# Kernel optimization log

Hardware: AMD Instinct MI355X
Metric: run time of the kernel (lower is better)

Reference implementation:

```python
import jax, jax.numpy as jnp
import numpy as np

DIM = 128
SQRT_DIM = float(np.sqrt(DIM))


def setup_inputs() -> dict:
    key = jax.random.key(0)
    k1, k2, k3, k4 = jax.random.split(key, 4)
    B, S, D = 16, 2048, DIM
    return {
        "query": jax.random.normal(k1, (B, S, D), dtype=jnp.float32),
        "key": jax.random.normal(k2, (B, S, D), dtype=jnp.float32),
        "value": jax.random.normal(k3, (B, S, D), dtype=jnp.float32),
        "trust_score": jax.random.uniform(k4, (B, 1, S), dtype=jnp.float32, minval=0.05, maxval=1.0),
    }


def reference(query, key, value, trust_score):
    # score: [B, q, k]
    score = jnp.einsum("bqd,bkd->bqk", query, key) / SQRT_DIM
    score = score * trust_score
    attn = jax.nn.softmax(score, axis=-1)
    # trust reweighting + renormalization
    attn = attn * trust_score
    attn = attn / jnp.sum(attn, axis=-1, keepdims=True)
    context = jnp.einsum("bqk,bkd->bqd", attn, value)
    return context
```

## Files before the change

kernel.cpp:

```cpp
#include <hip/hip_runtime.h>
#include <math.h>

#define SEQ 2048
#define DIM 128
#define KVB 32
#define NTILES (SEQ / KVB)
#define NT2 (NTILES / 2)
#define KTB 8192
#define VTB 8192

typedef __attribute__((ext_vector_type(8))) short bf16x8;
typedef __attribute__((ext_vector_type(16))) float f32x16;
typedef __attribute__((ext_vector_type(4))) short short4v;
typedef __attribute__((ext_vector_type(4))) float f32x4;

union frag_u { bf16x8 h; unsigned u[4]; };

__device__ __forceinline__ short f2bf(float f) {
  union { float f; unsigned u; } v; v.f = f;
  unsigned r = v.u + 0x7FFFu + ((v.u >> 16) & 1u);
  return (short)(r >> 16);
}
__device__ __forceinline__ float bf2f(short h) {
  return __uint_as_float(((unsigned)(unsigned short)h) << 16);
}
__device__ __forceinline__ void dma16(const void* g, void* l) {
  __builtin_amdgcn_global_load_lds(
      (const __attribute__((address_space(1))) void*)g,
      (__attribute__((address_space(3))) void*)l, 16, 0, 0);
}
__device__ __forceinline__ unsigned cvtpk(float lo, float hi) {
  unsigned r;
  asm("v_cvt_pk_bf16_f32 %0, %1, %2" : "=v"(r) : "v"(lo), "v"(hi));
  return r;
}
__device__ __forceinline__ void pl32swap(unsigned& a, unsigned& b) {
  asm("v_permlane32_swap_b32 %0, %1" : "+v"(a), "+v"(b));
}

__global__ __launch_bounds__(256)
void prepack_kernel(const float* __restrict__ Kg, const float* __restrict__ Vg,
                    const float* __restrict__ Tg,
                    char* __restrict__ Kws, char* __restrict__ Vws,
                    unsigned* __restrict__ Lws) {
  const int tile = blockIdx.x, b = blockIdx.y;
  const int tid = (int)threadIdx.x;
  const float* Kb = Kg + ((size_t)b * SEQ + tile * KVB) * DIM;
  const float* Vb = Vg + ((size_t)b * SEQ + tile * KVB) * DIM;
  const float* Tb = Tg + (size_t)b * SEQ + tile * KVB;
  char* kd = Kws + (size_t)(b * NTILES + tile) * KTB;
  char* vd = Vws + (size_t)(b * NTILES + tile) * VTB;

  #pragma unroll
  for (int i = 0; i < 2; ++i) {
    int id = i * 256 + tid;
    int k = id >> 4, c16 = id & 15;
    float sc = Tb[k] * 0.12751743f;
    const float4 f0 = *(const float4*)(Kb + (size_t)k * DIM + c16 * 8);
    const float4 f1 = *(const float4*)(Kb + (size_t)k * DIM + c16 * 8 + 4);
    bf16x8 pk;
    pk[0]=f2bf(f0.x*sc); pk[1]=f2bf(f0.y*sc); pk[2]=f2bf(f0.z*sc); pk[3]=f2bf(f0.w*sc);
    pk[4]=f2bf(f1.x*sc); pk[5]=f2bf(f1.y*sc); pk[6]=f2bf(f1.z*sc); pk[7]=f2bf(f1.w*sc);
    *(bf16x8*)(kd + k * 256 + ((c16 ^ (k & 7) ^ ((k >> 3) & 3)) << 4)) = pk;
  }
  #pragma unroll
  for (int i = 0; i < 2; ++i) {
    int id = i * 256 + tid;
    int d = id & 127, ch = id >> 7;
    const float* src = Vb + (size_t)(ch * 8) * DIM + d;
    bf16x8 pk;
    #pragma unroll
    for (int j = 0; j < 8; ++j) pk[j] = f2bf(src[(size_t)j * DIM]);
    *(bf16x8*)(vd + d * 64 + ((ch ^ ((d >> 1) & 3) ^ ((d >> 3) & 3)) << 4)) = pk;
  }
  if (tid < KVB) {
    float t = Tb[tid];
    float lt = log2f(t);
    short h = f2bf(lt);
    short lo = f2bf(lt - bf2f(h));
    Lws[(size_t)b * SEQ + tile * KVB + tid] =
        (unsigned)(unsigned short)h | ((unsigned)(unsigned short)lo << 16);
  }
}

__global__ __launch_bounds__(256, 2)
void trust_attn_main(const float* __restrict__ Qg, const char* __restrict__ Kws,
                     const char* __restrict__ Vws, const unsigned* __restrict__ Lws,
                     float* __restrict__ Og, int swz) {
  __shared__ __align__(16) char smem[65536];

  const int bid = (int)blockIdx.x;
  int b, qblk;
  if (swz) { int xcd = bid & 7, idx = bid >> 3; b = xcd * 2 + (idx >> 5); qblk = idx & 31; }
  else     { b = bid >> 5; qblk = bid & 31; }

  const int tid = (int)threadIdx.x;
  const int h   = tid >> 7;
  const int gq  = (tid >> 6) & 1;
  const int l   = tid & 63;
  const int hi  = l >> 5, l31 = l & 31;
  const int t128 = tid & 127;
  const int qcol = qblk * 64 + gq * 32 + l31;

  const float* Qr = Qg + ((size_t)b * SEQ + qcol) * DIM;
  const char* Kt = Kws + (size_t)(b * NTILES + h * NT2) * KTB;
  const char* Vt = Vws + (size_t)(b * NTILES + h * NT2) * VTB;
  const unsigned* Lb = Lws + (size_t)b * SEQ + h * (NT2 * KVB);

  frag_u qf[8];
  #pragma unroll
  for (int c = 0; c < 8; ++c) {
    const float4 a = *(const float4*)(Qr + c * 16 + hi * 8);
    const float4 d = *(const float4*)(Qr + c * 16 + hi * 8 + 4);
    bf16x8 q8;
    q8[0]=f2bf(a.x); q8[1]=f2bf(a.y); q8[2]=f2bf(a.z); q8[3]=f2bf(a.w);
    q8[4]=f2bf(d.x); q8[5]=f2bf(d.y); q8[6]=f2bf(d.z); q8[7]=f2bf(d.w);
    qf[c].h = q8;
  }
  frag_u qpad;
  qpad.u[0] = (hi == 0) ? 0x3F803F80u : 0u;
  qpad.u[1] = qpad.u[2] = qpad.u[3] = 0u;

  f32x16 acc[4];
  #pragma unroll
  for (int nt = 0; nt < 4; ++nt)
    #pragma unroll
    for (int i = 0; i < 16; ++i) acc[nt][i] = 0.f;
  float lsum = 0.f;

  auto ISSUE = [&](int t, int buf) {
    const char* ks = Kt + (size_t)t * KTB;
    const char* vs = Vt + (size_t)t * VTB;
    char* kl = smem + (h * 2 + buf) * 8192;
    char* vl = smem + 32768 + (h * 2 + buf) * 8192;
    #pragma unroll
    for (int j = 0; j < 2; ++j) {
      dma16(ks + j * 4096 + t128 * 16, kl + j * 4096 + t128 * 16);
      dma16(ks + j * 4096 + 2048 + t128 * 16, kl + j * 4096 + 2048 + t128 * 16);
      dma16(vs + j * 4096 + t128 * 16, vl + j * 4096 + t128 * 16);
      dma16(vs + j * 4096 + 2048 + t128 * 16, vl + j * 4096 + 2048 + t128 * 16);
    }
  };

  ISSUE(0, 0);
  unsigned ltc = Lb[l31];
  __syncthreads();

  for (int t = 0; t < NT2; ++t) {
    const int cur = t & 1;
    unsigned ltn = 0;
    if (t + 1 < NT2) {
      ISSUE(t + 1, cur ^ 1);
      ltn = Lb[(t + 1) * KVB + l31];
    }

    const char* Kc = smem + (h * 2 + cur) * 8192;
    const char* Vc = smem + 32768 + (h * 2 + cur) * 8192;

    f32x16 S0, S1;
    #pragma unroll
    for (int i = 0; i < 16; ++i) { S0[i] = 0.f; S1[i] = 0.f; }
    __builtin_amdgcn_s_setprio(1);
    #pragma unroll
    for (int c = 0; c < 8; c += 2) {
      frag_u kf0, kf1;
      kf0.h = *(const bf16x8*)(Kc + l31 * 256 + (((2 * c + hi) ^ (l31 & 7) ^ ((l31 >> 3) & 3)) << 4));
      kf1.h = *(const bf16x8*)(Kc + l31 * 256 + (((2 * (c + 1) + hi) ^ (l31 & 7) ^ ((l31 >> 3) & 3)) << 4));
      S0 = __builtin_amdgcn_mfma_f32_32x32x16_bf16(kf0.h, qf[c].h, S0, 0, 0, 0);
      S1 = __builtin_amdgcn_mfma_f32_32x32x16_bf16(kf1.h, qf[c + 1].h, S1, 0, 0, 0);
    }
    frag_u pa;
    pa.u[0] = (hi == 0) ? ltc : 0u;
    pa.u[1] = pa.u[2] = pa.u[3] = 0u;
    S1 = __builtin_amdgcn_mfma_f32_32x32x16_bf16(pa.h, qpad.h, S1, 0, 0, 0);
    __builtin_amdgcn_s_setprio(0);

    float p[16];
    #pragma unroll
    for (int i = 0; i < 16; ++i) {
      p[i] = __builtin_amdgcn_exp2f(S0[i] + S1[i]);
      lsum += p[i];
    }

    frag_u PA[2];
    #pragma unroll
    for (int ks = 0; ks < 2; ++ks) {
      unsigned a0 = cvtpk(p[8*ks+0], p[8*ks+1]);
      unsigned a1 = cvtpk(p[8*ks+2], p[8*ks+3]);
      unsigned b0 = cvtpk(p[8*ks+4], p[8*ks+5]);
      unsigned b1 = cvtpk(p[8*ks+6], p[8*ks+7]);
      pl32swap(a0, b0);
      pl32swap(a1, b1);
      PA[ks].u[0] = a0; PA[ks].u[1] = a1; PA[ks].u[2] = b0; PA[ks].u[3] = b1;
    }

    __builtin_amdgcn_s_setprio(1);
    #pragma unroll
    for (int nt = 0; nt < 4; ++nt)
      #pragma unroll
      for (int ks = 0; ks < 2; ++ks) {
        frag_u vf;
        vf.h = *(const bf16x8*)(Vc + (nt * 32 + l31) * 64 +
                (((2 * ks + hi) ^ ((l31 >> 1) & 3) ^ ((l31 >> 3) & 3)) << 4));
        acc[nt] = __builtin_amdgcn_mfma_f32_32x32x16_bf16(vf.h, PA[ks].h, acc[nt], 0, 0, 0);
      }
    __builtin_amdgcn_s_setprio(0);

    ltc = ltn;
    __syncthreads();
  }

  const float Z = lsum + __shfl_xor(lsum, 32);
  float* AccX = (float*)smem;
  float* Zx   = (float*)(smem + 32768);
  const int q2 = gq * 32 + l31;

  if (h == 1) {
    if (hi == 0) Zx[q2] = Z;
    #pragma unroll
    for (int nt = 0; nt < 4; ++nt)
      #pragma unroll
      for (int j = 0; j < 4; ++j) {
        int d = nt * 32 + j * 8 + hi * 4;
        int byte_off = (q2 * 512 + d * 4) ^ ((l31 & 7) << 4);
        f32x4 qd;
        qd[0] = acc[nt][j*4+0]; qd[1] = acc[nt][j*4+1];
        qd[2] = acc[nt][j*4+2]; qd[3] = acc[nt][j*4+3];
        *(f32x4*)((char*)AccX + byte_off) = qd;
      }
  }
  __syncthreads();
  if (h == 0) {
    const float inv = 1.0f / (Z + Zx[q2]);
    float* orow = Og + ((size_t)b * SEQ + qcol) * DIM;
    #pragma unroll
    for (int nt = 0; nt < 4; ++nt)
      #pragma unroll
      for (int j = 0; j < 4; ++j) {
        int d = nt * 32 + j * 8 + hi * 4;
        int byte_off = (q2 * 512 + d * 4) ^ ((l31 & 7) << 4);
        f32x4 o = *(const f32x4*)((const char*)AccX + byte_off);
        float4 r;
        r.x = (acc[nt][j*4+0] + o[0]) * inv;
        r.y = (acc[nt][j*4+1] + o[1]) * inv;
        r.z = (acc[nt][j*4+2] + o[2]) * inv;
        r.w = (acc[nt][j*4+3] + o[3]) * inv;
        *(float4*)(orow + d) = r;
      }
  }
}

__global__ __launch_bounds__(256, 2)
void trust_attn_fallback(const float* __restrict__ Qg, const float* __restrict__ Kg,
                         const float* __restrict__ Vg, const float* __restrict__ Tg,
                         float* __restrict__ Og) {
  __shared__ short Klds[2][64 * DIM];
  __shared__ short Vlds[2][DIM * 64];
  __shared__ short Plds[4][16 * 64];
  __shared__ float Tlds[2][64];

  const int b = blockIdx.y;
  const int qbase = blockIdx.x * 64;
  const int tid = (int)threadIdx.x;
  const int w = tid >> 6;
  const int l = tid & 63;
  const int lr = l & 15;
  const int lg = l >> 4;

  const float* Qb = Qg + (size_t)b * SEQ * DIM;
  const float* Kb = Kg + (size_t)b * SEQ * DIM;
  const float* Vb = Vg + (size_t)b * SEQ * DIM;
  const float* Tb = Tg + (size_t)b * SEQ;
  float*       Ob = Og + (size_t)b * SEQ * DIM;

  float4 kreg[8];
  float  vreg[32];
  float  treg;

  auto ISSUE = [&](int kv0) {
    #pragma unroll
    for (int i = 0; i < 8; ++i) {
      int flat4 = i * 256 + tid;
      int r = flat4 >> 5;
      int c4 = (flat4 & 31) << 2;
      kreg[i] = *(const float4*)(Kb + (size_t)(kv0 + r) * DIM + c4);
    }
    #pragma unroll
    for (int i = 0; i < 4; ++i) {
      int task = i * 256 + tid;
      int d = task & 127;
      int chunk = task >> 7;
      const float* src = Vb + (size_t)(kv0 + chunk * 8) * DIM + d;
      #pragma unroll
      for (int j = 0; j < 8; ++j) vreg[i * 8 + j] = src[(size_t)j * DIM];
    }
    treg = (tid < 64) ? Tb[kv0 + tid] : 0.f;
  };

  auto STORE = [&](int buf) {
    #pragma unroll
    for (int i = 0; i < 8; ++i) {
      int flat4 = i * 256 + tid;
      int r = flat4 >> 5;
      int c4 = (flat4 & 31) << 2;
      short4v pk;
      pk[0] = f2bf(kreg[i].x); pk[1] = f2bf(kreg[i].y);
      pk[2] = f2bf(kreg[i].z); pk[3] = f2bf(kreg[i].w);
      int byte_off = (r * 256 + (c4 << 1)) ^ ((r & 7) << 4);
      *(short4v*)((char*)&Klds[buf][0] + byte_off) = pk;
    }
    #pragma unroll
    for (int i = 0; i < 4; ++i) {
      int task = i * 256 + tid;
      int d = task & 127;
      int chunk = task >> 7;
      bf16x8 pk;
      #pragma unroll
      for (int j = 0; j < 8; ++j) pk[j] = f2bf(vreg[i * 8 + j]);
      int byte_off = (d * 128 + chunk * 16) ^ ((d & 7) << 4);
      *(bf16x8*)((char*)&Vlds[buf][0] + byte_off) = pk;
    }
    if (tid < 64) Tlds[buf][tid] = treg;
  };

  bf16x8 qf[4];
  {
    const float* qrow = Qb + (size_t)(qbase + w * 16 + lr) * DIM;
    #pragma unroll
    for (int kk = 0; kk < 4; ++kk) {
      const float4 a = *(const float4*)(qrow + kk * 32 + lg * 8);
      const float4 c = *(const float4*)(qrow + kk * 32 + lg * 8 + 4);
      bf16x8 f;
      f[0] = f2bf(a.x); f[1] = f2bf(a.y); f[2] = f2bf(a.z); f[3] = f2bf(a.w);
      f[4] = f2bf(c.x); f[5] = f2bf(c.y); f[6] = f2bf(c.z); f[7] = f2bf(c.w);
      qf[kk] = f;
    }
  }

  f32x4 acc[8];
  #pragma unroll
  for (int nt = 0; nt < 8; ++nt) acc[nt] = f32x4{0.f, 0.f, 0.f, 0.f};
  float lsum[4] = {0.f, 0.f, 0.f, 0.f};

  ISSUE(0);
  STORE(0);
  __syncthreads();

  for (int t = 0; t < SEQ / 64; ++t) {
    const int cur = t & 1;
    if (t + 1 < SEQ / 64) ISSUE((t + 1) * 64);

    const short* Kc = &Klds[cur][0];
    const short* Vc = &Vlds[cur][0];

    f32x4 s[4];
    #pragma unroll
    for (int kt = 0; kt < 4; ++kt) {
      f32x4 a0 = f32x4{0.f, 0.f, 0.f, 0.f};
      #pragma unroll
      for (int kk = 0; kk < 4; ++kk) {
        int row = kt * 16 + lr;
        int byte_off = (row * 256 + ((kk * 32 + lg * 8) << 1)) ^ ((row & 7) << 4);
        bf16x8 kf = *(const bf16x8*)((const char*)Kc + byte_off);
        a0 = __builtin_amdgcn_mfma_f32_16x16x32_bf16(qf[kk], kf, a0, 0, 0, 0);
      }
      s[kt] = a0;
    }

    short* Pw = Plds[w];
    #pragma unroll
    for (int kt = 0; kt < 4; ++kt) {
      float tt = Tlds[cur][kt * 16 + lr];
      float tc = tt * 0.12751743f;
      #pragma unroll
      for (int r = 0; r < 4; ++r) {
        float p = tt * exp2f(s[kt][r] * tc);
        lsum[r] += p;
        int q = lg * 4 + r;
        int byte_off = ((q * 128) + ((kt * 16 + lr) << 1)) ^ ((q & 7) << 4);
        *(short*)((char*)Pw + byte_off) = f2bf(p);
      }
    }
    asm volatile("s_waitcnt lgkmcnt(0)" ::: "memory");

    #pragma unroll
    for (int ks = 0; ks < 2; ++ks) {
      int byteA = (lr * 128 + ((ks * 32 + lg * 8) << 1)) ^ ((lr & 7) << 4);
      bf16x8 pf = *(const bf16x8*)((char*)Pw + byteA);
      #pragma unroll
      for (int nt = 0; nt < 8; ++nt) {
        int row = nt * 16 + lr;
        int byteB = (row * 128 + ((ks * 32 + lg * 8) << 1)) ^ ((row & 7) << 4);
        bf16x8 vf = *(const bf16x8*)((const char*)Vc + byteB);
        acc[nt] = __builtin_amdgcn_mfma_f32_16x16x32_bf16(pf, vf, acc[nt], 0, 0, 0);
      }
    }

    if (t + 1 < SEQ / 64) {
      STORE(cur ^ 1);
      __syncthreads();
    }
  }

  #pragma unroll
  for (int r = 0; r < 4; ++r) {
    float v = lsum[r];
    v += __shfl_xor(v, 1);
    v += __shfl_xor(v, 2);
    v += __shfl_xor(v, 4);
    v += __shfl_xor(v, 8);
    float inv = 1.0f / v;
    float* dst = Ob + (size_t)(qbase + w * 16 + lg * 4 + r) * DIM + lr;
    #pragma unroll
    for (int nt = 0; nt < 8; ++nt)
      dst[nt * 16] = acc[nt][r] * inv;
  }
}

extern "C" void kernel_launch(void* const* d_in, const int* in_sizes, int n_in,
                              void* d_out, int out_size, void* d_ws, size_t ws_size,
                              hipStream_t stream) {
  (void)n_in; (void)out_size;
  const float* Q = (const float*)d_in[0];
  const float* K = (const float*)d_in[1];
  const float* V = (const float*)d_in[2];
  const float* T = (const float*)d_in[3];
  float* O = (float*)d_out;
  const int B = in_sizes[0] / (SEQ * DIM);

  const size_t kv_bytes = (size_t)B * NTILES * KTB;
  const size_t need = kv_bytes * 2 + (size_t)B * SEQ * sizeof(unsigned);
  if (ws_size >= need) {
    char* Kws = (char*)d_ws;
    char* Vws = Kws + kv_bytes;
    unsigned* Lws = (unsigned*)(Vws + kv_bytes);
    dim3 gridp(NTILES, B);
    prepack_kernel<<<gridp, 256, 0, stream>>>(K, V, T, Kws, Vws, Lws);
    const int nblk = B * (SEQ / 64);
    const int swz = (B == 16) ? 1 : 0;
    trust_attn_main<<<nblk, 256, 0, stream>>>(Q, Kws, Vws, Lws, O, swz);
  } else {
    dim3 grid(SEQ / 64, B);
    trust_attn_fallback<<<grid, 256, 0, stream>>>(Q, K, V, T, O);
  }
}
```

Measured before the change: 66.27 us.

## Load K/V fragments directly from global into registers, dropping LDS staging

The prepack kernel now writes K and V in MFMA fragment order, so each lane's 16-byte fragment is contiguous. The main kernel reads those fragments straight from global memory into registers and prefetches the next tile during compute, replacing the LDS double buffer and per-tile __syncthreads. This removes LDS traffic and block-level barriers, but raises register pressure and exposes global-load latency. The two waves sharing a batch now each fetch the same K/V tiles from global/L2 rather than sharing them through LDS.

```diff
diff --git a/kernel.cpp b/kernel.cpp
--- a/kernel.cpp
+++ b/kernel.cpp
@@ -23,11 +23,6 @@
 }
 __device__ __forceinline__ float bf2f(short h) {
   return __uint_as_float(((unsigned)(unsigned short)h) << 16);
-}
-__device__ __forceinline__ void dma16(const void* g, void* l) {
-  __builtin_amdgcn_global_load_lds(
-      (const __attribute__((address_space(1))) void*)g,
-      (__attribute__((address_space(3))) void*)l, 16, 0, 0);
 }
 __device__ __forceinline__ unsigned cvtpk(float lo, float hi) {
   unsigned r;
@@ -54,24 +49,29 @@
   #pragma unroll
   for (int i = 0; i < 2; ++i) {
     int id = i * 256 + tid;
-    int k = id >> 4, c16 = id & 15;
+    int c = id >> 6, l = id & 63;
+    int hi = l >> 5, k = l & 31;
+    int dstart = (2 * c + hi) * 8;
     float sc = Tb[k] * 0.12751743f;
-    const float4 f0 = *(const float4*)(Kb + (size_t)k * DIM + c16 * 8);
-    const float4 f1 = *(const float4*)(Kb + (size_t)k * DIM + c16 * 8 + 4);
+    const float4 f0 = *(const float4*)(Kb + (size_t)k * DIM + dstart);
+    const float4 f1 = *(const float4*)(Kb + (size_t)k * DIM + dstart + 4);
     bf16x8 pk;
     pk[0]=f2bf(f0.x*sc); pk[1]=f2bf(f0.y*sc); pk[2]=f2bf(f0.z*sc); pk[3]=f2bf(f0.w*sc);
     pk[4]=f2bf(f1.x*sc); pk[5]=f2bf(f1.y*sc); pk[6]=f2bf(f1.z*sc); pk[7]=f2bf(f1.w*sc);
-    *(bf16x8*)(kd + k * 256 + ((c16 ^ (k & 7) ^ ((k >> 3) & 3)) << 4)) = pk;
+    *(bf16x8*)(kd + id * 16) = pk;
   }
   #pragma unroll
   for (int i = 0; i < 2; ++i) {
     int id = i * 256 + tid;
-    int d = id & 127, ch = id >> 7;
-    const float* src = Vb + (size_t)(ch * 8) * DIM + d;
+    int g = id >> 6, l = id & 63;
+    int hi = l >> 5, l31 = l & 31;
+    int d = (g >> 1) * 32 + l31;
+    int kstart = (2 * (g & 1) + hi) * 8;
+    const float* src = Vb + (size_t)kstart * DIM + d;
     bf16x8 pk;
     #pragma unroll
     for (int j = 0; j < 8; ++j) pk[j] = f2bf(src[(size_t)j * DIM]);
-    *(bf16x8*)(vd + d * 64 + ((ch ^ ((d >> 1) & 3) ^ ((d >> 3) & 3)) << 4)) = pk;
+    *(bf16x8*)(vd + id * 16) = pk;
   }
   if (tid < KVB) {
     float t = Tb[tid];
@@ -87,7 +87,7 @@
 void trust_attn_main(const float* __restrict__ Qg, const char* __restrict__ Kws,
                      const char* __restrict__ Vws, const unsigned* __restrict__ Lws,
                      float* __restrict__ Og, int swz) {
-  __shared__ __align__(16) char smem[65536];
+  __shared__ __align__(16) char smem[33280];
 
   const int bid = (int)blockIdx.x;
   int b, qblk;
@@ -99,12 +99,11 @@
   const int gq  = (tid >> 6) & 1;
   const int l   = tid & 63;
   const int hi  = l >> 5, l31 = l & 31;
-  const int t128 = tid & 127;
   const int qcol = qblk * 64 + gq * 32 + l31;
 
   const float* Qr = Qg + ((size_t)b * SEQ + qcol) * DIM;
-  const char* Kt = Kws + (size_t)(b * NTILES + h * NT2) * KTB;
-  const char* Vt = Vws + (size_t)(b * NTILES + h * NT2) * VTB;
+  const char* Kt = Kws + (size_t)(b * NTILES + h * NT2) * KTB + l * 16;
+  const char* Vt = Vws + (size_t)(b * NTILES + h * NT2) * VTB + l * 16;
   const unsigned* Lb = Lws + (size_t)b * SEQ + h * (NT2 * KVB);
 
   frag_u qf[8];
@@ -128,34 +127,16 @@
     for (int i = 0; i < 16; ++i) acc[nt][i] = 0.f;
   float lsum = 0.f;
 
-  auto ISSUE = [&](int t, int buf) {
-    const char* ks = Kt + (size_t)t * KTB;
-    const char* vs = Vt + (size_t)t * VTB;
-    char* kl = smem + (h * 2 + buf) * 8192;
-    char* vl = smem + 32768 + (h * 2 + buf) * 8192;
-    #pragma unroll
-    for (int j = 0; j < 2; ++j) {
-      dma16(ks + j * 4096 + t128 * 16, kl + j * 4096 + t128 * 16);
-      dma16(ks + j * 4096 + 2048 + t128 * 16, kl + j * 4096 + 2048 + t128 * 16);
-      dma16(vs + j * 4096 + t128 * 16, vl + j * 4096 + t128 * 16);
-      dma16(vs + j * 4096 + 2048 + t128 * 16, vl + j * 4096 + 2048 + t128 * 16);
-    }
-  };
-
-  ISSUE(0, 0);
+  frag_u kf[8], vf[8];
+  #pragma unroll
+  for (int c = 0; c < 8; ++c) kf[c].h = *(const bf16x8*)(Kt + c * 1024);
+  #pragma unroll
+  for (int g = 0; g < 8; ++g) vf[g].h = *(const bf16x8*)(Vt + g * 1024);
   unsigned ltc = Lb[l31];
-  __syncthreads();
 
   for (int t = 0; t < NT2; ++t) {
-    const int cur = t & 1;
-    unsigned ltn = 0;
-    if (t + 1 < NT2) {
-      ISSUE(t + 1, cur ^ 1);
-      ltn = Lb[(t + 1) * KVB + l31];
-    }
-
-    const char* Kc = smem + (h * 2 + cur) * 8192;
-    const char* Vc = smem + 32768 + (h * 2 + cur) * 8192;
+    const char* Kn = Kt + (size_t)(t + 1) * KTB;
+    const char* Vn = Vt + (size_t)(t + 1) * VTB;
 
     f32x16 S0, S1;
     #pragma unroll
@@ -163,17 +144,21 @@
     __builtin_amdgcn_s_setprio(1);
     #pragma unroll
     for (int c = 0; c < 8; c += 2) {
-      frag_u kf0, kf1;
-      kf0.h = *(const bf16x8*)(Kc + l31 * 256 + (((2 * c + hi) ^ (l31 & 7) ^ ((l31 >> 3) & 3)) << 4));
-      kf1.h = *(const bf16x8*)(Kc + l31 * 256 + (((2 * (c + 1) + hi) ^ (l31 & 7) ^ ((l31 >> 3) & 3)) << 4));
-      S0 = __builtin_amdgcn_mfma_f32_32x32x16_bf16(kf0.h, qf[c].h, S0, 0, 0, 0);
-      S1 = __builtin_amdgcn_mfma_f32_32x32x16_bf16(kf1.h, qf[c + 1].h, S1, 0, 0, 0);
+      S0 = __builtin_amdgcn_mfma_f32_32x32x16_bf16(kf[c].h, qf[c].h, S0, 0, 0, 0);
+      S1 = __builtin_amdgcn_mfma_f32_32x32x16_bf16(kf[c + 1].h, qf[c + 1].h, S1, 0, 0, 0);
     }
     frag_u pa;
     pa.u[0] = (hi == 0) ? ltc : 0u;
     pa.u[1] = pa.u[2] = pa.u[3] = 0u;
     S1 = __builtin_amdgcn_mfma_f32_32x32x16_bf16(pa.h, qpad.h, S1, 0, 0, 0);
     __builtin_amdgcn_s_setprio(0);
+
+    unsigned ltn = 0;
+    if (t + 1 < NT2) {
+      #pragma unroll
+      for (int c = 0; c < 8; ++c) kf[c].h = *(const bf16x8*)(Kn + c * 1024);
+      ltn = Lb[(t + 1) * KVB + l31];
+    }
 
     float p[16];
     #pragma unroll
@@ -198,16 +183,15 @@
     #pragma unroll
     for (int nt = 0; nt < 4; ++nt)
       #pragma unroll
-      for (int ks = 0; ks < 2; ++ks) {
-        frag_u vf;
-        vf.h = *(const bf16x8*)(Vc + (nt * 32 + l31) * 64 +
-                (((2 * ks + hi) ^ ((l31 >> 1) & 3) ^ ((l31 >> 3) & 3)) << 4));
-        acc[nt] = __builtin_amdgcn_mfma_f32_32x32x16_bf16(vf.h, PA[ks].h, acc[nt], 0, 0, 0);
-      }
+      for (int ks = 0; ks < 2; ++ks)
+        acc[nt] = __builtin_amdgcn_mfma_f32_32x32x16_bf16(vf[nt * 2 + ks].h, PA[ks].h, acc[nt], 0, 0, 0);
     __builtin_amdgcn_s_setprio(0);
 
+    if (t + 1 < NT2) {
+      #pragma unroll
+      for (int g = 0; g < 8; ++g) vf[g].h = *(const bf16x8*)(Vn + g * 1024);
+    }
     ltc = ltn;
-    __syncthreads();
   }
 
   const float Z = lsum + __shfl_xor(lsum, 32);
@@ -215,6 +199,7 @@
   float* Zx   = (float*)(smem + 32768);
   const int q2 = gq * 32 + l31;
 
+  __syncthreads();
   if (h == 1) {
     if (hi == 0) Zx[q2] = Z;
     #pragma unroll
```

Result: no change. 67.55 us (+1.9%).
